# Kernel optimization log

Hardware: AMD Instinct MI355X
Metric: run time of the kernel (lower is better)

The kernel has to match this reference:

```python
import jax, jax.numpy as jnp
import numpy as np

N, E, H, F = 50000, 400000, 128, 64
INV_SQRT_3 = 1.0 / np.sqrt(3.0)
INV_SQRT_H = 1.0 / np.sqrt(H)
SILU_SCALE = 1.0 / 0.6  # ScaledSiLU


def setup_inputs() -> dict:
    key = jax.random.key(0)
    ks = jax.random.split(key, 16)
    inp = {
        "x": jax.random.normal(ks[0], (N, H), jnp.float32),
        "x_defect": jax.random.normal(ks[1], (N, H), jnp.float32),
        "vec": jax.random.normal(ks[2], (N, 3, H), jnp.float32),
        "edge_feat": jax.random.normal(ks[3], (E, F), jnp.float32),
        "edge_vector": jax.random.normal(ks[4], (E, 3), jnp.float32),
        "edge_index": jax.random.randint(ks[5], (2, E), 0, N, jnp.int64)
        if jax.config.jax_enable_x64 else jax.random.randint(ks[5], (2, E), 0, N, jnp.int32),
        # parameters (Linear weights stored as [in, out])
        "W_defect": jax.random.normal(ks[6], (H, 3 * H), jnp.float32) / np.sqrt(H),
        "b_defect": jnp.zeros((3 * H,), jnp.float32),
        "W_x1": jax.random.normal(ks[7], (H, H // 2), jnp.float32) / np.sqrt(H),
        "b_x1": jnp.zeros((H // 2,), jnp.float32),
        "W_x2": jax.random.normal(ks[8], (H // 2, 3 * H), jnp.float32) / np.sqrt(H // 2),
        "b_x2": jnp.zeros((3 * H,), jnp.float32),
        "W_edge": jax.random.normal(ks[9], (F, 3 * H), jnp.float32) / np.sqrt(F),
        "b_edge": jnp.zeros((3 * H,), jnp.float32),
        "W_lvec": jax.random.normal(ks[10], (H, H), jnp.float32) / np.sqrt(H),
        "W_gvec": jax.random.normal(ks[11], (H, 1), jnp.float32) / np.sqrt(H),
    }
    return inp


def _vector_activation(v, W_lvec, W_gvec):
    # v: [N, 3, H]
    gvec = v @ W_gvec                      # [N, 3, 1]
    lvec = v @ W_lvec                      # [N, 3, H]
    dotprod = (lvec * gvec).sum(1, keepdims=True)  # [N, 1, H]
    mask = (dotprod >= 0).astype(v.dtype)
    return mask * lvec + (1 - mask) * (lvec + gvec) * 0.5


def reference(x, x_defect, vec, edge_feat, edge_vector, edge_index,
              W_defect, b_defect, W_x1, b_x1, W_x2, b_x2,
              W_edge, b_edge, W_lvec, W_gvec):
    j, i = edge_index[0], edge_index[1]
    rbf_h = edge_feat @ W_edge + b_edge                        # [E, 3H]
    xd = x_defect @ W_defect + b_defect                        # [N, 3H]
    h1 = jax.nn.silu(x @ W_x1 + b_x1) * SILU_SCALE             # ScaledSiLU
    xh = h1 @ W_x2 + b_x2                                      # [N, 3H]

    msg = xh[j] * (xd[j] + xd[i]) * rbf_h * INV_SQRT_3         # [E, 3H]
    x_ji1, x_ji2, x_ji3 = jnp.split(msg, 3, axis=-1)           # each [E, H]

    vec_ji = (x_ji1[:, None, :] * vec[j]
              + x_ji2[:, None, :] * edge_vector[:, :, None]) * INV_SQRT_H  # [E,3,H]

    d_vec = jax.ops.segment_sum(vec_ji, i, num_segments=x.shape[0])  # [N,3,H]
    d_vec = _vector_activation(d_vec, W_lvec, W_gvec)
    d_x = jax.ops.segment_sum(x_ji3, i, num_segments=x.shape[0])     # [N,H]
    return (d_x, d_vec)
```

## Files before the change

### kernel.cpp

```cpp
#include <hip/hip_runtime.h>
#include <math.h>

#define NN 50000
#define EE 400000

__global__ __launch_bounds__(256) void k_h1(
    const float* __restrict__ x, const float* __restrict__ W,
    const float* __restrict__ b, float* __restrict__ h1)
{
    __shared__ float xs[32 * 128];
    int t = threadIdx.x;
    int base = blockIdx.x * 32;
    const float4* xv = (const float4*)x;
    for (int idx = t; idx < 1024; idx += 256) {
        int r = idx >> 5, c = idx & 31;
        int row = base + r; if (row >= NN) row = NN - 1;
        ((float4*)xs)[r * 32 + c] = xv[(size_t)row * 32 + c];
    }
    __syncthreads();
    int c = t & 63, rr = t >> 6;
    float acc[8] = {};
    for (int k = 0; k < 128; ++k) {
        float wv = W[k * 64 + c];
        #pragma unroll
        for (int q = 0; q < 8; ++q) acc[q] += xs[(rr + 4 * q) * 128 + k] * wv;
    }
    float bb = b[c];
    #pragma unroll
    for (int q = 0; q < 8; ++q) {
        int row = base + rr + 4 * q;
        if (row < NN) {
            float z = acc[q] + bb;
            h1[(size_t)row * 64 + c] = z / (1.f + expf(-z)) * (1.f / 0.6f);
        }
    }
}

template <int K>
__global__ __launch_bounds__(256) void k_gemm384(
    const float* __restrict__ A, const float* __restrict__ W,
    const float* __restrict__ b, float* __restrict__ out)
{
    __shared__ float as[32 * K];
    int t = threadIdx.x;
    int base = blockIdx.x * 32;
    const float4* av = (const float4*)A;
    const int K4 = K / 4;
    for (int idx = t; idx < 32 * K4; idx += 256) {
        int r = idx / K4, c = idx % K4;
        int row = base + r; if (row >= NN) row = NN - 1;
        ((float4*)as)[r * K4 + c] = av[(size_t)row * K4 + c];
    }
    __syncthreads();
    int c = t & 63, rr = t >> 6;
    float acc[8][6] = {};
    for (int k = 0; k < K; ++k) {
        float wv[6];
        #pragma unroll
        for (int m = 0; m < 6; ++m) wv[m] = W[k * 384 + c + 64 * m];
        #pragma unroll
        for (int q = 0; q < 8; ++q) {
            float a = as[(rr + 4 * q) * K + k];
            #pragma unroll
            for (int m = 0; m < 6; ++m) acc[q][m] += a * wv[m];
        }
    }
    float bb[6];
    #pragma unroll
    for (int m = 0; m < 6; ++m) bb[m] = b[c + 64 * m];
    #pragma unroll
    for (int q = 0; q < 8; ++q) {
        int row = base + rr + 4 * q;
        if (row < NN) {
            #pragma unroll
            for (int m = 0; m < 6; ++m)
                out[(size_t)row * 384 + c + 64 * m] = acc[q][m] + bb[m];
        }
    }
}

__global__ __launch_bounds__(256) void k_edge(
    const float* __restrict__ ef, const float* __restrict__ ev,
    const int* __restrict__ eidx,
    const float* __restrict__ We, const float* __restrict__ be,
    const float* __restrict__ xd, const float* __restrict__ xh,
    const float* __restrict__ vec,
    float* __restrict__ dx, float* __restrict__ dvec)
{
    __shared__ float efs[32 * 64];
    __shared__ float evs[96];
    __shared__ int js[32], is_[32];
    int t = threadIdx.x;
    int ebase = blockIdx.x * 32;
    const float4* efv = (const float4*)ef;
    for (int idx = t; idx < 512; idx += 256)
        ((float4*)efs)[idx] = efv[(size_t)ebase * 16 + idx];
    if (t < 32) { js[t] = eidx[ebase + t]; is_[t] = eidx[(size_t)EE + ebase + t]; }
    if (t < 96) evs[t] = ev[(size_t)ebase * 3 + t];
    __syncthreads();
    int c = t & 63, w = t >> 6;
    float acc[8][6] = {};
    for (int k = 0; k < 64; ++k) {
        float wv[6];
        #pragma unroll
        for (int m = 0; m < 6; ++m) wv[m] = We[k * 384 + c + 64 * m];
        #pragma unroll
        for (int r = 0; r < 8; ++r) {
            float f = efs[(4 * r + w) * 64 + k];
            #pragma unroll
            for (int m = 0; m < 6; ++m) acc[r][m] += f * wv[m];
        }
    }
    float bb[6];
    #pragma unroll
    for (int m = 0; m < 6; ++m) bb[m] = be[c + 64 * m];
    const float IS3 = 0.57735026918962576f;
    const float ISH = 0.08838834764831845f;
    for (int r = 0; r < 8; ++r) {
        int e = 4 * r + w;
        int j = js[e], i = is_[e];
        size_t jb = (size_t)j * 384, ib = (size_t)i * 384;
        float msg[6];
        #pragma unroll
        for (int m = 0; m < 6; ++m) {
            int col = c + 64 * m;
            float rbf = acc[r][m] + bb[m];
            float xdv = xd[jb + col] + xd[ib + col];
            msg[m] = xh[jb + col] * xdv * rbf * IS3;
        }
        #pragma unroll
        for (int d = 0; d < 3; ++d) {
            float ed = evs[e * 3 + d];
            float v0 = vec[jb + d * 128 + c];
            float v1 = vec[jb + d * 128 + c + 64];
            unsafeAtomicAdd(&dvec[ib + d * 128 + c],      (msg[0] * v0 + msg[2] * ed) * ISH);
            unsafeAtomicAdd(&dvec[ib + d * 128 + c + 64], (msg[1] * v1 + msg[3] * ed) * ISH);
        }
        unsafeAtomicAdd(&dx[(size_t)i * 128 + c],      msg[4]);
        unsafeAtomicAdd(&dx[(size_t)i * 128 + c + 64], msg[5]);
    }
}

__global__ __launch_bounds__(256) void k_act(
    float* vio, const float* __restrict__ Wl, const float* __restrict__ Wg)
{
    __shared__ float vs[4 * 384];
    __shared__ float wg[128];
    int t = threadIdx.x;
    if (t < 128) wg[t] = Wg[t];
    int w = t >> 6, l = t & 63;
    for (int it = 0; it < 4; ++it) {
        __syncthreads();
        int nb = blockIdx.x * 16 + it * 4;
        const float4* vsrc = (const float4*)(vio + (size_t)nb * 384);
        float4* vdst = (float4*)vs;
        for (int idx = t; idx < 384; idx += 256) vdst[idx] = vsrc[idx];
        __syncthreads();
        const float* v = &vs[w * 384];
        float g0 = v[l] * wg[l] + v[l + 64] * wg[l + 64];
        float g1 = v[128 + l] * wg[l] + v[128 + l + 64] * wg[l + 64];
        float g2 = v[256 + l] * wg[l] + v[256 + l + 64] * wg[l + 64];
        #pragma unroll
        for (int off = 32; off > 0; off >>= 1) {
            g0 += __shfl_xor(g0, off, 64);
            g1 += __shfl_xor(g1, off, 64);
            g2 += __shfl_xor(g2, off, 64);
        }
        float a[3][2] = {};
        #pragma unroll 4
        for (int h = 0; h < 128; ++h) {
            float w0 = Wl[h * 128 + l];
            float w1 = Wl[h * 128 + l + 64];
            float v0 = v[h], v1 = v[128 + h], v2 = v[256 + h];
            a[0][0] += v0 * w0; a[0][1] += v0 * w1;
            a[1][0] += v1 * w0; a[1][1] += v1 * w1;
            a[2][0] += v2 * w0; a[2][1] += v2 * w1;
        }
        int node = nb + w;
        size_t ob = (size_t)node * 384;
        float gv[3] = { g0, g1, g2 };
        #pragma unroll
        for (int cc = 0; cc < 2; ++cc) {
            int col = l + 64 * cc;
            float dot = a[0][cc] * g0 + a[1][cc] * g1 + a[2][cc] * g2;
            bool m = dot >= 0.f;
            #pragma unroll
            for (int d = 0; d < 3; ++d) {
                float lv = a[d][cc];
                vio[ob + d * 128 + col] = m ? lv : 0.5f * (lv + gv[d]);
            }
        }
    }
}

extern "C" void kernel_launch(void* const* d_in, const int* in_sizes, int n_in,
                              void* d_out, int out_size, void* d_ws, size_t ws_size,
                              hipStream_t stream)
{
    const float* x   = (const float*)d_in[0];
    const float* xde = (const float*)d_in[1];
    const float* vec = (const float*)d_in[2];
    const float* ef  = (const float*)d_in[3];
    const float* ev  = (const float*)d_in[4];
    const int*   eidx= (const int*)d_in[5];
    const float* Wd  = (const float*)d_in[6];
    const float* bd  = (const float*)d_in[7];
    const float* W1  = (const float*)d_in[8];
    const float* b1  = (const float*)d_in[9];
    const float* W2  = (const float*)d_in[10];
    const float* b2  = (const float*)d_in[11];
    const float* We  = (const float*)d_in[12];
    const float* be  = (const float*)d_in[13];
    const float* Wl  = (const float*)d_in[14];
    const float* Wg  = (const float*)d_in[15];

    float* xd = (float*)d_ws;
    float* xh = xd + (size_t)NN * 384;
    float* h1 = (float*)d_out;
    float* dx   = (float*)d_out;
    float* dvec = dx + (size_t)NN * 128;

    k_h1<<<1563, 256, 0, stream>>>(x, W1, b1, h1);
    k_gemm384<128><<<1563, 256, 0, stream>>>(xde, Wd, bd, xd);
    k_gemm384<64><<<1563, 256, 0, stream>>>(h1, W2, b2, xh);
    hipMemsetAsync(d_out, 0, (size_t)out_size * sizeof(float), stream);
    k_edge<<<12500, 256, 0, stream>>>(ef, ev, eidx, We, be, xd, xh, vec, dx, dvec);
    k_act<<<3125, 256, 0, stream>>>(dvec, Wl, Wg);
}
```

Baseline: 1.216 ms.

## Sort edges by destination and combine atomics for same-destination runs

Builds a counting sort of edges by destination node (histogram, single-block scan, scatter into a permutation) every call. The edge kernel then processes edges in sorted order, with each wavefront handling 8 consecutive edges. It accumulates contributions in registers while the destination stays the same and issues atomics only when the destination changes. This targets atomic traffic and contention on dvec/dx. The cost is three extra kernels, including a serial single-block scan, plus gathered (non-contiguous) loads of edge features.

```diff
diff --git a/kernel.cpp b/kernel.cpp
--- a/kernel.cpp
+++ b/kernel.cpp
@@ -3,6 +3,7 @@
 
 #define NN 50000
 #define EE 400000
+#define NBINS 50176
 
 __global__ __launch_bounds__(256) void k_h1(
     const float* __restrict__ x, const float* __restrict__ W,
@@ -79,9 +80,48 @@
     }
 }
 
-__global__ __launch_bounds__(256) void k_edge(
+__global__ __launch_bounds__(256) void k_hist(
+    const int* __restrict__ eidx, int* __restrict__ cnt)
+{
+    int e = blockIdx.x * 256 + threadIdx.x;
+    if (e < EE) atomicAdd(&cnt[eidx[(size_t)EE + e]], 1);
+}
+
+__global__ __launch_bounds__(1024) void k_scan(
+    const int* __restrict__ cnt, int* __restrict__ off2)
+{
+    __shared__ int part[1024];
+    int t = threadIdx.x;
+    int base = t * 49;
+    int s = 0;
+    #pragma unroll 7
+    for (int q = 0; q < 49; ++q) s += cnt[base + q];
+    part[t] = s;
+    __syncthreads();
+    int mine = s;
+    for (int d = 1; d < 1024; d <<= 1) {
+        int v = (t >= d) ? part[t - d] : 0;
+        __syncthreads();
+        part[t] += v;
+        __syncthreads();
+    }
+    int run = part[t] - mine;
+    for (int q = 0; q < 49; ++q) { off2[base + q] = run; run += cnt[base + q]; }
+}
+
+__global__ __launch_bounds__(256) void k_scatter(
+    const int* __restrict__ eidx, int* __restrict__ off2, int* __restrict__ perm)
+{
+    int e = blockIdx.x * 256 + threadIdx.x;
+    if (e < EE) {
+        int pos = atomicAdd(&off2[eidx[(size_t)EE + e]], 1);
+        perm[pos] = e;
+    }
+}
+
+__global__ __launch_bounds__(256) void k_edge_sorted(
     const float* __restrict__ ef, const float* __restrict__ ev,
-    const int* __restrict__ eidx,
+    const int* __restrict__ eidx, const int* __restrict__ perm,
     const float* __restrict__ We, const float* __restrict__ be,
     const float* __restrict__ xd, const float* __restrict__ xh,
     const float* __restrict__ vec,
@@ -89,15 +129,26 @@
 {
     __shared__ float efs[32 * 64];
     __shared__ float evs[96];
+    __shared__ int perm_s[32];
     __shared__ int js[32], is_[32];
     int t = threadIdx.x;
     int ebase = blockIdx.x * 32;
+    if (t < 32) perm_s[t] = perm[ebase + t];
+    __syncthreads();
+    if (t < 32) { int e = perm_s[t]; js[t] = eidx[e]; is_[t] = eidx[(size_t)EE + e]; }
+    if (t >= 128 && t < 224) {
+        int q = t - 128;
+        int e = perm_s[q / 3];
+        evs[q] = ev[(size_t)e * 3 + q % 3];
+    }
     const float4* efv = (const float4*)ef;
-    for (int idx = t; idx < 512; idx += 256)
-        ((float4*)efs)[idx] = efv[(size_t)ebase * 16 + idx];
-    if (t < 32) { js[t] = eidx[ebase + t]; is_[t] = eidx[(size_t)EE + ebase + t]; }
-    if (t < 96) evs[t] = ev[(size_t)ebase * 3 + t];
-    __syncthreads();
+    for (int idx = t; idx < 512; idx += 256) {
+        int r = idx >> 4;
+        int e = perm_s[r];
+        ((float4*)efs)[idx] = efv[(size_t)e * 16 + (idx & 15)];
+    }
+    __syncthreads();
+
     int c = t & 63, w = t >> 6;
     float acc[8][6] = {};
     for (int k = 0; k < 64; ++k) {
@@ -106,7 +157,7 @@
         for (int m = 0; m < 6; ++m) wv[m] = We[k * 384 + c + 64 * m];
         #pragma unroll
         for (int r = 0; r < 8; ++r) {
-            float f = efs[(4 * r + w) * 64 + k];
+            float f = efs[(8 * w + r) * 64 + k];
             #pragma unroll
             for (int m = 0; m < 6; ++m) acc[r][m] += f * wv[m];
         }
@@ -114,11 +165,16 @@
     float bb[6];
     #pragma unroll
     for (int m = 0; m < 6; ++m) bb[m] = be[c + 64 * m];
+
     const float IS3 = 0.57735026918962576f;
     const float ISH = 0.08838834764831845f;
+
+    int curI = -1;
+    float s[8];
+    #pragma unroll
     for (int r = 0; r < 8; ++r) {
-        int e = 4 * r + w;
-        int j = js[e], i = is_[e];
+        int eL = 8 * w + r;
+        int j = js[eL], i = is_[eL];
         size_t jb = (size_t)j * 384, ib = (size_t)i * 384;
         float msg[6];
         #pragma unroll
@@ -128,16 +184,47 @@
             float xdv = xd[jb + col] + xd[ib + col];
             msg[m] = xh[jb + col] * xdv * rbf * IS3;
         }
+        float cb[8];
         #pragma unroll
         for (int d = 0; d < 3; ++d) {
-            float ed = evs[e * 3 + d];
+            float ed = evs[eL * 3 + d];
             float v0 = vec[jb + d * 128 + c];
             float v1 = vec[jb + d * 128 + c + 64];
-            unsafeAtomicAdd(&dvec[ib + d * 128 + c],      (msg[0] * v0 + msg[2] * ed) * ISH);
-            unsafeAtomicAdd(&dvec[ib + d * 128 + c + 64], (msg[1] * v1 + msg[3] * ed) * ISH);
-        }
-        unsafeAtomicAdd(&dx[(size_t)i * 128 + c],      msg[4]);
-        unsafeAtomicAdd(&dx[(size_t)i * 128 + c + 64], msg[5]);
+            cb[2 * d]     = (msg[0] * v0 + msg[2] * ed) * ISH;
+            cb[2 * d + 1] = (msg[1] * v1 + msg[3] * ed) * ISH;
+        }
+        cb[6] = msg[4]; cb[7] = msg[5];
+
+        if (i != curI) {
+            if (curI >= 0) {
+                size_t pb = (size_t)curI * 384;
+                unsafeAtomicAdd(&dvec[pb + 0 * 128 + c],      s[0]);
+                unsafeAtomicAdd(&dvec[pb + 0 * 128 + c + 64], s[1]);
+                unsafeAtomicAdd(&dvec[pb + 1 * 128 + c],      s[2]);
+                unsafeAtomicAdd(&dvec[pb + 1 * 128 + c + 64], s[3]);
+                unsafeAtomicAdd(&dvec[pb + 2 * 128 + c],      s[4]);
+                unsafeAtomicAdd(&dvec[pb + 2 * 128 + c + 64], s[5]);
+                unsafeAtomicAdd(&dx[(size_t)curI * 128 + c],      s[6]);
+                unsafeAtomicAdd(&dx[(size_t)curI * 128 + c + 64], s[7]);
+            }
+            curI = i;
+            #pragma unroll
+            for (int q = 0; q < 8; ++q) s[q] = cb[q];
+        } else {
+            #pragma unroll
+            for (int q = 0; q < 8; ++q) s[q] += cb[q];
+        }
+    }
+    {
+        size_t pb = (size_t)curI * 384;
+        unsafeAtomicAdd(&dvec[pb + 0 * 128 + c],      s[0]);
+        unsafeAtomicAdd(&dvec[pb + 0 * 128 + c + 64], s[1]);
+        unsafeAtomicAdd(&dvec[pb + 1 * 128 + c],      s[2]);
+        unsafeAtomicAdd(&dvec[pb + 1 * 128 + c + 64], s[3]);
+        unsafeAtomicAdd(&dvec[pb + 2 * 128 + c],      s[4]);
+        unsafeAtomicAdd(&dvec[pb + 2 * 128 + c + 64], s[5]);
+        unsafeAtomicAdd(&dx[(size_t)curI * 128 + c],      s[6]);
+        unsafeAtomicAdd(&dx[(size_t)curI * 128 + c + 64], s[7]);
     }
 }
 
@@ -214,16 +301,24 @@
     const float* Wl  = (const float*)d_in[14];
     const float* Wg  = (const float*)d_in[15];
 
-    float* xd = (float*)d_ws;
-    float* xh = xd + (size_t)NN * 384;
-    float* h1 = (float*)d_out;
+    float* xd  = (float*)d_ws;
+    float* xh  = xd + (size_t)NN * 384;
+    int* cnt   = (int*)(xh + (size_t)NN * 384);
+    int* off2  = cnt + NBINS;
+    int* perm  = off2 + NBINS;
+    float* h1  = (float*)d_out;
     float* dx   = (float*)d_out;
     float* dvec = dx + (size_t)NN * 128;
+
+    hipMemsetAsync(cnt, 0, NBINS * sizeof(int), stream);
+    k_hist<<<1563, 256, 0, stream>>>(eidx, cnt);
+    k_scan<<<1, 1024, 0, stream>>>(cnt, off2);
+    k_scatter<<<1563, 256, 0, stream>>>(eidx, off2, perm);
 
     k_h1<<<1563, 256, 0, stream>>>(x, W1, b1, h1);
     k_gemm384<128><<<1563, 256, 0, stream>>>(xde, Wd, bd, xd);
     k_gemm384<64><<<1563, 256, 0, stream>>>(h1, W2, b2, xh);
     hipMemsetAsync(d_out, 0, (size_t)out_size * sizeof(float), stream);
-    k_edge<<<12500, 256, 0, stream>>>(ef, ev, eidx, We, be, xd, xh, vec, dx, dvec);
+    k_edge_sorted<<<12500, 256, 0, stream>>>(ef, ev, eidx, perm, We, be, xd, xh, vec, dx, dvec);
     k_act<<<3125, 256, 0, stream>>>(dvec, Wl, Wg);
 }
```

Result: faster. 1.013 ms (-16.7%).
